# Kernel optimization log

Hardware: AMD Instinct MI355X
Metric: run time of the kernel (lower is better)

The kernel has to match this reference:

```python
import jax, jax.numpy as jnp
import numpy as np

G = 5000      # n_genes (nodes)
IN = 64       # in_dim
D = 128       # embed_dims
E = 240000    # edges (before self-loops)
SLOPE = 0.2   # leakyrelu_slope (outer) and GATv2 internal negative_slope (PyG default 0.2)


def setup_inputs() -> dict:
    key = jax.random.key(0)
    ks = jax.random.split(key, 12)
    s = 0.05
    return {
        "x": jax.random.normal(ks[0], (G, IN), jnp.float32),
        "edge_index": jax.random.randint(ks[1], (2, E), 0, G, jnp.int64),
        # per-gene input linears: n_genes independent Linear(in_dim -> embed_dims)
        "W_in": jax.random.normal(ks[2], (G, IN, D), jnp.float32) * s,
        "b_in": jnp.zeros((G, D), jnp.float32),
        # GATv2Conv params (heads=1): lin_l, lin_r, att, bias
        "W_l": jax.random.normal(ks[3], (D, D), jnp.float32) * s,
        "b_l": jnp.zeros((D,), jnp.float32),
        "W_r": jax.random.normal(ks[4], (D, D), jnp.float32) * s,
        "b_r": jnp.zeros((D,), jnp.float32),
        "att": jax.random.normal(ks[5], (D,), jnp.float32) * s,
        "bias": jnp.zeros((D,), jnp.float32),
        # output MLP: Linear(D*G -> D), Linear(D -> 1)
        "W1": jax.random.normal(ks[6], (D * G, D), jnp.float32) * 0.001,
        "b1": jnp.zeros((D,), jnp.float32),
        "W2": jax.random.normal(ks[7], (D, 1), jnp.float32) * s,
        "b2": jnp.zeros((1,), jnp.float32),
    }


def _leaky(v, slope):
    return jnp.where(v >= 0, v, slope * v)


def reference(x, edge_index, W_in, b_in, W_l, b_l, W_r, b_r, att, bias, W1, b1, W2, b2):
    # per-gene linear + relu: [G, IN] x [G, IN, D] -> [G, D]
    h = jax.nn.relu(jnp.einsum("gi,gid->gd", x, W_in) + b_in)

    # GATv2Conv (heads=1, concat, add_self_loops=True)
    xl = h @ W_l + b_l  # source-side transform [G, D]
    xr = h @ W_r + b_r  # target-side transform [G, D]
    loop = jnp.arange(G, dtype=edge_index.dtype)
    src = jnp.concatenate([edge_index[0], loop])  # [E+G]
    dst = jnp.concatenate([edge_index[1], loop])

    # attention logits per edge: att . LeakyReLU(xl[src] + xr[dst])
    e = _leaky(xl[src] + xr[dst], 0.2) @ att  # [E+G]

    # segment softmax over edges sharing a destination
    m = jax.ops.segment_max(e, dst, num_segments=G)  # [G]
    w = jnp.exp(e - m[dst])
    z = jax.ops.segment_sum(w, dst, num_segments=G)  # [G]
    alpha = w / z[dst]  # every node has a self-loop, z > 0

    # scatter-aggregate weighted messages
    out = jax.ops.segment_sum(alpha[:, None] * xl[src], dst, num_segments=G) + bias  # [G, D]

    out = _leaky(out, SLOPE)
    flat = out.reshape(-1)  # [G*D]
    h1 = jax.nn.relu(flat @ W1 + b1)
    return h1 @ W2 + b2  # [1]
```

## Files before the change

### kernel.cpp

```cpp
#include <hip/hip_runtime.h>
#include <math.h>

#define G 5000
#define IN 64
#define D 128
#define E 240000
#define EG (E + G)
#define SLOPE 0.2f
#define GD (G * D)
#define CAP 128
#define NB_M 1250
#define NB_PG 1250
#define NB_H 240
#define NB_X 1250

__device__ __forceinline__ float leaky(float v) { return v >= 0.f ? v : SLOPE * v; }

__global__ __launch_bounds__(256) void k_fuseA(const float* __restrict__ x,
                                               const float* __restrict__ Win,
                                               const float* __restrict__ bin,
                                               float* __restrict__ h,
                                               const int* __restrict__ srcA,
                                               const int* __restrict__ dstA,
                                               int* __restrict__ cnt,
                                               int* __restrict__ ssrc,
                                               float* __restrict__ outz) {
    if (blockIdx.x == 0 && threadIdx.x == 0) *outz = 0.f;
    if (blockIdx.x < NB_PG) {
        int g = (blockIdx.x * 256 + threadIdx.x) >> 6;
        int lane = threadIdx.x & 63;
        if (g >= G) return;
        float xv = x[g * IN + lane];
        const float* W = Win + (size_t)g * IN * D + lane * 2;
        float2 acc = *(const float2*)(bin + g * D + lane * 2);
#pragma unroll
        for (int i = 0; i < IN; ++i) {
            float xi = __shfl(xv, i);
            float2 w2 = *(const float2*)(W + (size_t)i * D);
            acc.x = fmaf(xi, w2.x, acc.x);
            acc.y = fmaf(xi, w2.y, acc.y);
        }
        float2 o = { fmaxf(acc.x, 0.f), fmaxf(acc.y, 0.f) };
        *(float2*)(h + g * D + lane * 2) = o;
    } else {
        int base = ((blockIdx.x - NB_PG) * 256 + threadIdx.x) * 4;
        if (base >= EG) return;
        if (base + 4 <= E) {
            int4 s4 = *(const int4*)(srcA + base);
            int4 d4 = *(const int4*)(dstA + base);
            int p;
            p = atomicAdd(&cnt[d4.x], 1); if (p < CAP) ssrc[d4.x * CAP + p] = s4.x;
            p = atomicAdd(&cnt[d4.y], 1); if (p < CAP) ssrc[d4.y * CAP + p] = s4.y;
            p = atomicAdd(&cnt[d4.z], 1); if (p < CAP) ssrc[d4.z * CAP + p] = s4.z;
            p = atomicAdd(&cnt[d4.w], 1); if (p < CAP) ssrc[d4.w * CAP + p] = s4.w;
        } else {
            for (int kk = 0; kk < 4; ++kk) {
                int i = base + kk;
                if (i < EG) {
                    int s, t;
                    if (i < E) { s = srcA[i]; t = dstA[i]; }
                    else { s = i - E; t = s; }
                    int p = atomicAdd(&cnt[t], 1);
                    if (p < CAP) ssrc[t * CAP + p] = s;
                }
            }
        }
    }
}

__global__ __launch_bounds__(256) void k_xlxr3(const float* __restrict__ h,
                                               const float* __restrict__ Wl,
                                               const float* __restrict__ bl,
                                               const float* __restrict__ Wr,
                                               const float* __restrict__ br,
                                               float* __restrict__ xl,
                                               float* __restrict__ xr) {
    int g0 = blockIdx.x * 4;
    int tid = threadIdx.x;
    int half = tid >> 7;
    int col = tid & 127;
    const float* W = half ? Wr : Wl;
    const float* bb = half ? br : bl;
    float* o = half ? xr : xl;
    const float* h0p = h + (size_t)(g0 + 0) * D;
    const float* h1p = h + (size_t)(g0 + 1) * D;
    const float* h2p = h + (size_t)(g0 + 2) * D;
    const float* h3p = h + (size_t)(g0 + 3) * D;
    float b = bb[col];
    float acc0 = b, acc1 = b, acc2 = b, acc3 = b;
#pragma unroll 8
    for (int k4 = 0; k4 < 32; ++k4) {
        int k = k4 * 4;
        float4 hv0 = *(const float4*)(h0p + k);
        float4 hv1 = *(const float4*)(h1p + k);
        float4 hv2 = *(const float4*)(h2p + k);
        float4 hv3 = *(const float4*)(h3p + k);
        float w0 = W[(size_t)(k + 0) * D + col];
        float w1 = W[(size_t)(k + 1) * D + col];
        float w2 = W[(size_t)(k + 2) * D + col];
        float w3 = W[(size_t)(k + 3) * D + col];
        acc0 = fmaf(hv0.x, w0, acc0); acc0 = fmaf(hv0.y, w1, acc0);
        acc0 = fmaf(hv0.z, w2, acc0); acc0 = fmaf(hv0.w, w3, acc0);
        acc1 = fmaf(hv1.x, w0, acc1); acc1 = fmaf(hv1.y, w1, acc1);
        acc1 = fmaf(hv1.z, w2, acc1); acc1 = fmaf(hv1.w, w3, acc1);
        acc2 = fmaf(hv2.x, w0, acc2); acc2 = fmaf(hv2.y, w1, acc2);
        acc2 = fmaf(hv2.z, w2, acc2); acc2 = fmaf(hv2.w, w3, acc2);
        acc3 = fmaf(hv3.x, w0, acc3); acc3 = fmaf(hv3.y, w1, acc3);
        acc3 = fmaf(hv3.z, w2, acc3); acc3 = fmaf(hv3.w, w3, acc3);
    }
    o[(size_t)(g0 + 0) * D + col] = acc0;
    o[(size_t)(g0 + 1) * D + col] = acc1;
    o[(size_t)(g0 + 2) * D + col] = acc2;
    o[(size_t)(g0 + 3) * D + col] = acc3;
}

__global__ __launch_bounds__(256) void k_aggmlp(const int* __restrict__ cnt,
                                                const int* __restrict__ ssrc,
                                                const float* __restrict__ xl,
                                                const float* __restrict__ xr,
                                                const float* __restrict__ att,
                                                const float* __restrict__ bias,
                                                const float* __restrict__ W1,
                                                float* __restrict__ partials) {
    int wid = threadIdx.x >> 6;
    int lane = threadIdx.x & 63;
    int t = __builtin_amdgcn_readfirstlane(blockIdx.x * 4 + wid);
    __shared__ float2 red[4][64];
    int lane2 = lane * 2;
    float2 a  = *(const float2*)(att + lane2);
    float2 r2 = *(const float2*)(xr + (size_t)t * D + lane2);
    int deg = cnt[t]; if (deg > CAP) deg = CAP;
    const int* srow = ssrc + t * CAP;
    float2 acc = { 0.f, 0.f };
    float z = 0.f;
    for (int base = 0; base < deg; base += 64) {
        int nv = deg - base; if (nv > 64) nv = 64;
        int sv = srow[base + (lane < nv ? lane : nv - 1)];
        int e = 0;
        for (; e + 4 <= nv; e += 4) {
            int s0 = __shfl(sv, e), s1 = __shfl(sv, e + 1);
            int s2 = __shfl(sv, e + 2), s3 = __shfl(sv, e + 3);
            float2 l0 = *(const float2*)(xl + (size_t)s0 * D + lane2);
            float2 l1 = *(const float2*)(xl + (size_t)s1 * D + lane2);
            float2 l2 = *(const float2*)(xl + (size_t)s2 * D + lane2);
            float2 l3 = *(const float2*)(xl + (size_t)s3 * D + lane2);
            float v0 = leaky(l0.x + r2.x) * a.x + leaky(l0.y + r2.y) * a.y;
            float v1 = leaky(l1.x + r2.x) * a.x + leaky(l1.y + r2.y) * a.y;
            float v2 = leaky(l2.x + r2.x) * a.x + leaky(l2.y + r2.y) * a.y;
            float v3 = leaky(l3.x + r2.x) * a.x + leaky(l3.y + r2.y) * a.y;
#pragma unroll
            for (int off = 32; off; off >>= 1) {
                v0 += __shfl_xor(v0, off);
                v1 += __shfl_xor(v1, off);
                v2 += __shfl_xor(v2, off);
                v3 += __shfl_xor(v3, off);
            }
            float w0 = expf(v0), w1 = expf(v1), w2 = expf(v2), w3 = expf(v3);
            z += (w0 + w1) + (w2 + w3);
            acc.x = fmaf(w0, l0.x, acc.x); acc.y = fmaf(w0, l0.y, acc.y);
            acc.x = fmaf(w1, l1.x, acc.x); acc.y = fmaf(w1, l1.y, acc.y);
            acc.x = fmaf(w2, l2.x, acc.x); acc.y = fmaf(w2, l2.y, acc.y);
            acc.x = fmaf(w3, l3.x, acc.x); acc.y = fmaf(w3, l3.y, acc.y);
        }
        for (; e < nv; ++e) {
            int s = __shfl(sv, e);
            float2 l = *(const float2*)(xl + (size_t)s * D + lane2);
            float v = leaky(l.x + r2.x) * a.x + leaky(l.y + r2.y) * a.y;
#pragma unroll
            for (int off = 32; off; off >>= 1) v += __shfl_xor(v, off);
            float w = expf(v);
            z += w;
            acc.x = fmaf(w, l.x, acc.x);
            acc.y = fmaf(w, l.y, acc.y);
        }
    }
    float inv = 1.f / z;
    float2 bv = *(const float2*)(bias + lane2);
    float2 o = { leaky(acc.x * inv + bv.x), leaky(acc.y * inv + bv.y) };

    const float* W1p = W1 + (size_t)t * D * D + lane2;
    float2 m = { 0.f, 0.f };
#pragma unroll 8
    for (int dp = 0; dp < 64; ++dp) {
        float fx = __shfl(o.x, dp);
        float fy = __shfl(o.y, dp);
        float2 wa = *(const float2*)(W1p + (size_t)(2 * dp) * D);
        float2 wb = *(const float2*)(W1p + (size_t)(2 * dp + 1) * D);
        m.x = fmaf(fx, wa.x, m.x); m.y = fmaf(fx, wa.y, m.y);
        m.x = fmaf(fy, wb.x, m.x); m.y = fmaf(fy, wb.y, m.y);
    }
    red[wid][lane] = m;
    __syncthreads();
    if (wid == 0) {
        float2 s0 = red[0][lane], s1 = red[1][lane], s2 = red[2][lane], s3 = red[3][lane];
        float2 s = { s0.x + s1.x + s2.x + s3.x, s0.y + s1.y + s2.y + s3.y };
        *(float2*)(partials + (size_t)blockIdx.x * D + lane2) = s;
    }
}

__global__ __launch_bounds__(1024) void k_final8(const float* __restrict__ partials,
                                                 const float* __restrict__ b1,
                                                 const float* __restrict__ W2,
                                                 const float* __restrict__ b2,
                                                 float* __restrict__ out) {
    int tid = threadIdx.x;
    int rg = tid >> 4;
    int cl = tid & 15;
    int c = blockIdx.x * 16 + cl;
    float s = 0.f;
    for (int r = rg; r < NB_M; r += 64) s += partials[(size_t)r * D + c];
    __shared__ float red[64][16];
    red[rg][cl] = s;
    __syncthreads();
    if (tid < 128) {
        int cc = tid & 15, seg = tid >> 4;
        float t2 = red[seg * 8][cc];
        for (int m = 1; m < 8; ++m) t2 += red[seg * 8 + m][cc];
        red[seg * 8][cc] = t2;
    }
    __syncthreads();
    if (tid < 16) {
        float tot = 0.f;
        for (int m = 0; m < 8; ++m) tot += red[m * 8][tid];
        float h1 = fmaxf(tot + b1[blockIdx.x * 16 + tid], 0.f);
        red[0][tid] = h1 * W2[blockIdx.x * 16 + tid];
    }
    __syncthreads();
    if (tid == 0) {
        float o = 0.f;
        for (int m = 0; m < 16; ++m) o += red[0][m];
        if (blockIdx.x == 0) o += b2[0];
        atomicAdd(out, o);
    }
}

extern "C" void kernel_launch(void* const* d_in, const int* in_sizes, int n_in,
                              void* d_out, int out_size, void* d_ws, size_t ws_size,
                              hipStream_t stream) {
    const float* x    = (const float*)d_in[0];
    const int*   ei   = (const int*)d_in[1];
    const float* Win  = (const float*)d_in[2];
    const float* bin  = (const float*)d_in[3];
    const float* Wl   = (const float*)d_in[4];
    const float* bl   = (const float*)d_in[5];
    const float* Wr   = (const float*)d_in[6];
    const float* br   = (const float*)d_in[7];
    const float* att  = (const float*)d_in[8];
    const float* bias = (const float*)d_in[9];
    const float* W1   = (const float*)d_in[10];
    const float* b1   = (const float*)d_in[11];
    const float* W2   = (const float*)d_in[12];
    const float* b2   = (const float*)d_in[13];
    float* out = (float*)d_out;

    float* ws       = (float*)d_ws;
    float* h        = ws;
    float* xl       = h  + GD;
    float* xr       = xl + GD;
    float* partials = xr + GD;
    int*   ssrc     = (int*)(partials + (size_t)NB_M * D);
    int*   cnt      = ssrc + (size_t)G * CAP;

    const int* srcA = ei;
    const int* dstA = ei + E;

    hipMemsetAsync(cnt, 0, G * sizeof(int), stream);
    k_fuseA<<<NB_PG + NB_H, 256, 0, stream>>>(x, Win, bin, h, srcA, dstA, cnt, ssrc, out);
    k_xlxr3<<<NB_X, 256, 0, stream>>>(h, Wl, bl, Wr, br, xl, xr);
    k_aggmlp<<<NB_M, 256, 0, stream>>>(cnt, ssrc, xl, xr, att, bias, W1, partials);
    k_final8<<<8, 1024, 0, stream>>>(partials, b1, W2, b2, out);
}
```

Before: 140.9 us.

## Split each node's edge aggregation across a full block and prefetch W1 into registers

Launches one block per node instead of one wave per node, giving each wave up to 64 of the node's edges and combining the partial softmax sums and accumulators through shared memory. Each wave loads its 32 rows of W1 into registers at the start, so the large W1 stream overlaps with the edge gather. The W1 product is split across waves by row, and a per-node partial vector is written out. This raises parallelism and memory-level concurrency, at the cost of more registers, extra block syncs and a larger partials buffer that the final reduction must sum over all nodes.

```diff
diff --git a/kernel.cpp b/kernel.cpp
--- a/kernel.cpp
+++ b/kernel.cpp
@@ -9,7 +9,6 @@
 #define SLOPE 0.2f
 #define GD (G * D)
 #define CAP 128
-#define NB_M 1250
 #define NB_PG 1250
 #define NB_H 240
 #define NB_X 1250
@@ -114,26 +113,33 @@
     o[(size_t)(g0 + 3) * D + col] = acc3;
 }
 
-__global__ __launch_bounds__(256) void k_aggmlp(const int* __restrict__ cnt,
-                                                const int* __restrict__ ssrc,
-                                                const float* __restrict__ xl,
-                                                const float* __restrict__ xr,
-                                                const float* __restrict__ att,
-                                                const float* __restrict__ bias,
-                                                const float* __restrict__ W1,
-                                                float* __restrict__ partials) {
+__global__ __launch_bounds__(256) void k_aggmlp2(const int* __restrict__ cnt,
+                                                 const int* __restrict__ ssrc,
+                                                 const float* __restrict__ xl,
+                                                 const float* __restrict__ xr,
+                                                 const float* __restrict__ att,
+                                                 const float* __restrict__ bias,
+                                                 const float* __restrict__ W1,
+                                                 float* __restrict__ partials) {
     int wid = threadIdx.x >> 6;
     int lane = threadIdx.x & 63;
-    int t = __builtin_amdgcn_readfirstlane(blockIdx.x * 4 + wid);
-    __shared__ float2 red[4][64];
+    int t = blockIdx.x;
     int lane2 = lane * 2;
+
+    const float* W1base = W1 + ((size_t)t * D + wid * 32) * D + lane2;
+    float2 w1reg[32];
+#pragma unroll
+    for (int r = 0; r < 32; ++r)
+        w1reg[r] = *(const float2*)(W1base + (size_t)r * D);
+
     float2 a  = *(const float2*)(att + lane2);
     float2 r2 = *(const float2*)(xr + (size_t)t * D + lane2);
     int deg = cnt[t]; if (deg > CAP) deg = CAP;
     const int* srow = ssrc + t * CAP;
     float2 acc = { 0.f, 0.f };
     float z = 0.f;
-    for (int base = 0; base < deg; base += 64) {
+    int base = wid * 64;
+    if (base < deg) {
         int nv = deg - base; if (nv > 64) nv = 64;
         int sv = srow[base + (lane < nv ? lane : nv - 1)];
         int e = 0;
@@ -174,27 +180,34 @@
             acc.y = fmaf(w, l.y, acc.y);
         }
     }
-    float inv = 1.f / z;
+
+    __shared__ float2 red[4][64];
+    __shared__ float zs[4];
+    red[wid][lane] = acc;
+    if (lane == 0) zs[wid] = z;
+    __syncthreads();
+    float2 s0 = red[0][lane], s1 = red[1][lane], s2 = red[2][lane], s3 = red[3][lane];
+    float2 atot = { s0.x + s1.x + s2.x + s3.x, s0.y + s1.y + s2.y + s3.y };
+    float zt = zs[0] + zs[1] + zs[2] + zs[3];
+    float inv = 1.f / zt;
     float2 bv = *(const float2*)(bias + lane2);
-    float2 o = { leaky(acc.x * inv + bv.x), leaky(acc.y * inv + bv.y) };
-
-    const float* W1p = W1 + (size_t)t * D * D + lane2;
+    float2 o = { leaky(atot.x * inv + bv.x), leaky(atot.y * inv + bv.y) };
+
     float2 m = { 0.f, 0.f };
-#pragma unroll 8
-    for (int dp = 0; dp < 64; ++dp) {
-        float fx = __shfl(o.x, dp);
-        float fy = __shfl(o.y, dp);
-        float2 wa = *(const float2*)(W1p + (size_t)(2 * dp) * D);
-        float2 wb = *(const float2*)(W1p + (size_t)(2 * dp + 1) * D);
-        m.x = fmaf(fx, wa.x, m.x); m.y = fmaf(fx, wa.y, m.y);
-        m.x = fmaf(fy, wb.x, m.x); m.y = fmaf(fy, wb.y, m.y);
-    }
+#pragma unroll
+    for (int rp = 0; rp < 16; ++rp) {
+        float fx = __shfl(o.x, wid * 16 + rp);
+        float fy = __shfl(o.y, wid * 16 + rp);
+        m.x = fmaf(fx, w1reg[2 * rp].x, m.x);     m.y = fmaf(fx, w1reg[2 * rp].y, m.y);
+        m.x = fmaf(fy, w1reg[2 * rp + 1].x, m.x); m.y = fmaf(fy, w1reg[2 * rp + 1].y, m.y);
+    }
+    __syncthreads();
     red[wid][lane] = m;
     __syncthreads();
     if (wid == 0) {
-        float2 s0 = red[0][lane], s1 = red[1][lane], s2 = red[2][lane], s3 = red[3][lane];
-        float2 s = { s0.x + s1.x + s2.x + s3.x, s0.y + s1.y + s2.y + s3.y };
-        *(float2*)(partials + (size_t)blockIdx.x * D + lane2) = s;
+        float2 m0 = red[0][lane], m1 = red[1][lane], m2 = red[2][lane], m3 = red[3][lane];
+        float2 s = { m0.x + m1.x + m2.x + m3.x, m0.y + m1.y + m2.y + m3.y };
+        *(float2*)(partials + (size_t)t * D + lane2) = s;
     }
 }
 
@@ -208,7 +221,7 @@
     int cl = tid & 15;
     int c = blockIdx.x * 16 + cl;
     float s = 0.f;
-    for (int r = rg; r < NB_M; r += 64) s += partials[(size_t)r * D + c];
+    for (int r = rg; r < G; r += 64) s += partials[(size_t)r * D + c];
     __shared__ float red[64][16];
     red[rg][cl] = s;
     __syncthreads();
@@ -258,7 +271,7 @@
     float* xl       = h  + GD;
     float* xr       = xl + GD;
     float* partials = xr + GD;
-    int*   ssrc     = (int*)(partials + (size_t)NB_M * D);
+    int*   ssrc     = (int*)(partials + (size_t)GD);
     int*   cnt      = ssrc + (size_t)G * CAP;
 
     const int* srcA = ei;
@@ -267,6 +280,6 @@
     hipMemsetAsync(cnt, 0, G * sizeof(int), stream);
     k_fuseA<<<NB_PG + NB_H, 256, 0, stream>>>(x, Win, bin, h, srcA, dstA, cnt, ssrc, out);
     k_xlxr3<<<NB_X, 256, 0, stream>>>(h, Wl, bl, Wr, br, xl, xr);
-    k_aggmlp<<<NB_M, 256, 0, stream>>>(cnt, ssrc, xl, xr, att, bias, W1, partials);
+    k_aggmlp2<<<G, 256, 0, stream>>>(cnt, ssrc, xl, xr, att, bias, W1, partials);
     k_final8<<<8, 1024, 0, stream>>>(partials, b1, W2, b2, out);
 }
```

New measurement: 184.6 us. 1.31x slower.

## Split aggregation: precompute first half of nodes in separate kernel

Applied to the files above, without the earlier changes.

The GATv2 attention aggregation for the first 2500 nodes moves into a new kernel that writes its features to a workspace buffer. The fused aggregation+W1 kernel then reads those features and only does the gather and softmax for the second half. The intent is to shorten the combined kernel, where the gather latency and the W1 streaming compete, and to balance work across waves. The cost is an extra launch and an extra 2.5 MB write and read of intermediate features.

```diff
diff --git a/kernel.cpp b/kernel.cpp
--- a/kernel.cpp
+++ b/kernel.cpp
@@ -9,12 +9,73 @@
 #define SLOPE 0.2f
 #define GD (G * D)
 #define CAP 128
+#define HALF 2500
 #define NB_M 1250
 #define NB_PG 1250
 #define NB_H 240
 #define NB_X 1250
 
 __device__ __forceinline__ float leaky(float v) { return v >= 0.f ? v : SLOPE * v; }
+
+__device__ __forceinline__ float2 agg_butterfly(int t, int lane, int lane2,
+                                                const int* __restrict__ cnt,
+                                                const int* __restrict__ ssrc,
+                                                const float* __restrict__ xl,
+                                                const float* __restrict__ xr,
+                                                const float* __restrict__ att,
+                                                const float* __restrict__ bias) {
+    float2 a  = *(const float2*)(att + lane2);
+    float2 r2 = *(const float2*)(xr + (size_t)t * D + lane2);
+    int deg = cnt[t]; if (deg > CAP) deg = CAP;
+    const int* srow = ssrc + t * CAP;
+    float2 acc = { 0.f, 0.f };
+    float z = 0.f;
+    for (int base = 0; base < deg; base += 64) {
+        int nv = deg - base; if (nv > 64) nv = 64;
+        int sv = srow[base + (lane < nv ? lane : nv - 1)];
+        int e = 0;
+        for (; e + 4 <= nv; e += 4) {
+            int s0 = __shfl(sv, e), s1 = __shfl(sv, e + 1);
+            int s2 = __shfl(sv, e + 2), s3 = __shfl(sv, e + 3);
+            float2 l0 = *(const float2*)(xl + (size_t)s0 * D + lane2);
+            float2 l1 = *(const float2*)(xl + (size_t)s1 * D + lane2);
+            float2 l2 = *(const float2*)(xl + (size_t)s2 * D + lane2);
+            float2 l3 = *(const float2*)(xl + (size_t)s3 * D + lane2);
+            float v0 = leaky(l0.x + r2.x) * a.x + leaky(l0.y + r2.y) * a.y;
+            float v1 = leaky(l1.x + r2.x) * a.x + leaky(l1.y + r2.y) * a.y;
+            float v2 = leaky(l2.x + r2.x) * a.x + leaky(l2.y + r2.y) * a.y;
+            float v3 = leaky(l3.x + r2.x) * a.x + leaky(l3.y + r2.y) * a.y;
+#pragma unroll
+            for (int off = 32; off; off >>= 1) {
+                v0 += __shfl_xor(v0, off);
+                v1 += __shfl_xor(v1, off);
+                v2 += __shfl_xor(v2, off);
+                v3 += __shfl_xor(v3, off);
+            }
+            float w0 = expf(v0), w1 = expf(v1), w2 = expf(v2), w3 = expf(v3);
+            z += (w0 + w1) + (w2 + w3);
+            acc.x = fmaf(w0, l0.x, acc.x); acc.y = fmaf(w0, l0.y, acc.y);
+            acc.x = fmaf(w1, l1.x, acc.x); acc.y = fmaf(w1, l1.y, acc.y);
+            acc.x = fmaf(w2, l2.x, acc.x); acc.y = fmaf(w2, l2.y, acc.y);
+            acc.x = fmaf(w3, l3.x, acc.x); acc.y = fmaf(w3, l3.y, acc.y);
+        }
+        for (; e < nv; ++e) {
+            int s = __shfl(sv, e);
+            float2 l = *(const float2*)(xl + (size_t)s * D + lane2);
+            float v = leaky(l.x + r2.x) * a.x + leaky(l.y + r2.y) * a.y;
+#pragma unroll
+            for (int off = 32; off; off >>= 1) v += __shfl_xor(v, off);
+            float w = expf(v);
+            z += w;
+            acc.x = fmaf(w, l.x, acc.x);
+            acc.y = fmaf(w, l.y, acc.y);
+        }
+    }
+    float inv = 1.f / z;
+    float2 bv = *(const float2*)(bias + lane2);
+    float2 o = { leaky(acc.x * inv + bv.x), leaky(acc.y * inv + bv.y) };
+    return o;
+}
 
 __global__ __launch_bounds__(256) void k_fuseA(const float* __restrict__ x,
                                                const float* __restrict__ Win,
@@ -114,69 +175,41 @@
     o[(size_t)(g0 + 3) * D + col] = acc3;
 }
 
-__global__ __launch_bounds__(256) void k_aggmlp(const int* __restrict__ cnt,
-                                                const int* __restrict__ ssrc,
-                                                const float* __restrict__ xl,
-                                                const float* __restrict__ xr,
-                                                const float* __restrict__ att,
-                                                const float* __restrict__ bias,
-                                                const float* __restrict__ W1,
-                                                float* __restrict__ partials) {
+__global__ __launch_bounds__(256) void k_agg(const int* __restrict__ cnt,
+                                             const int* __restrict__ ssrc,
+                                             const float* __restrict__ xl,
+                                             const float* __restrict__ xr,
+                                             const float* __restrict__ att,
+                                             const float* __restrict__ bias,
+                                             float* __restrict__ f) {
+    int t = (blockIdx.x * 256 + threadIdx.x) >> 6;
+    int lane = threadIdx.x & 63;
+    if (t >= HALF) return;
+    float2 o = agg_butterfly(t, lane, lane * 2, cnt, ssrc, xl, xr, att, bias);
+    *(float2*)(f + (size_t)t * D + lane * 2) = o;
+}
+
+__global__ __launch_bounds__(256) void k_aggmlp5(const int* __restrict__ cnt,
+                                                 const int* __restrict__ ssrc,
+                                                 const float* __restrict__ xl,
+                                                 const float* __restrict__ xr,
+                                                 const float* __restrict__ att,
+                                                 const float* __restrict__ bias,
+                                                 const float* __restrict__ f,
+                                                 const float* __restrict__ W1,
+                                                 float* __restrict__ partials) {
     int wid = threadIdx.x >> 6;
     int lane = threadIdx.x & 63;
     int t = __builtin_amdgcn_readfirstlane(blockIdx.x * 4 + wid);
     __shared__ float2 red[4][64];
     int lane2 = lane * 2;
-    float2 a  = *(const float2*)(att + lane2);
-    float2 r2 = *(const float2*)(xr + (size_t)t * D + lane2);
-    int deg = cnt[t]; if (deg > CAP) deg = CAP;
-    const int* srow = ssrc + t * CAP;
-    float2 acc = { 0.f, 0.f };
-    float z = 0.f;
-    for (int base = 0; base < deg; base += 64) {
-        int nv = deg - base; if (nv > 64) nv = 64;
-        int sv = srow[base + (lane < nv ? lane : nv - 1)];
-        int e = 0;
-        for (; e + 4 <= nv; e += 4) {
-            int s0 = __shfl(sv, e), s1 = __shfl(sv, e + 1);
-            int s2 = __shfl(sv, e + 2), s3 = __shfl(sv, e + 3);
-            float2 l0 = *(const float2*)(xl + (size_t)s0 * D + lane2);
-            float2 l1 = *(const float2*)(xl + (size_t)s1 * D + lane2);
-            float2 l2 = *(const float2*)(xl + (size_t)s2 * D + lane2);
-            float2 l3 = *(const float2*)(xl + (size_t)s3 * D + lane2);
-            float v0 = leaky(l0.x + r2.x) * a.x + leaky(l0.y + r2.y) * a.y;
-            float v1 = leaky(l1.x + r2.x) * a.x + leaky(l1.y + r2.y) * a.y;
-            float v2 = leaky(l2.x + r2.x) * a.x + leaky(l2.y + r2.y) * a.y;
-            float v3 = leaky(l3.x + r2.x) * a.x + leaky(l3.y + r2.y) * a.y;
-#pragma unroll
-            for (int off = 32; off; off >>= 1) {
-                v0 += __shfl_xor(v0, off);
-                v1 += __shfl_xor(v1, off);
-                v2 += __shfl_xor(v2, off);
-                v3 += __shfl_xor(v3, off);
-            }
-            float w0 = expf(v0), w1 = expf(v1), w2 = expf(v2), w3 = expf(v3);
-            z += (w0 + w1) + (w2 + w3);
-            acc.x = fmaf(w0, l0.x, acc.x); acc.y = fmaf(w0, l0.y, acc.y);
-            acc.x = fmaf(w1, l1.x, acc.x); acc.y = fmaf(w1, l1.y, acc.y);
-            acc.x = fmaf(w2, l2.x, acc.x); acc.y = fmaf(w2, l2.y, acc.y);
-            acc.x = fmaf(w3, l3.x, acc.x); acc.y = fmaf(w3, l3.y, acc.y);
-        }
-        for (; e < nv; ++e) {
-            int s = __shfl(sv, e);
-            float2 l = *(const float2*)(xl + (size_t)s * D + lane2);
-            float v = leaky(l.x + r2.x) * a.x + leaky(l.y + r2.y) * a.y;
-#pragma unroll
-            for (int off = 32; off; off >>= 1) v += __shfl_xor(v, off);
-            float w = expf(v);
-            z += w;
-            acc.x = fmaf(w, l.x, acc.x);
-            acc.y = fmaf(w, l.y, acc.y);
-        }
-    }
-    float inv = 1.f / z;
-    float2 bv = *(const float2*)(bias + lane2);
-    float2 o = { leaky(acc.x * inv + bv.x), leaky(acc.y * inv + bv.y) };
+
+    float2 o;
+    if (t < HALF) {
+        o = *(const float2*)(f + (size_t)t * D + lane2);
+    } else {
+        o = agg_butterfly(t, lane, lane2, cnt, ssrc, xl, xr, att, bias);
+    }
 
     const float* W1p = W1 + (size_t)t * D * D + lane2;
     float2 m = { 0.f, 0.f };
@@ -257,7 +290,8 @@
     float* h        = ws;
     float* xl       = h  + GD;
     float* xr       = xl + GD;
-    float* partials = xr + GD;
+    float* f        = xr + GD;
+    float* partials = f  + GD;
     int*   ssrc     = (int*)(partials + (size_t)NB_M * D);
     int*   cnt      = ssrc + (size_t)G * CAP;
 
@@ -267,6 +301,7 @@
     hipMemsetAsync(cnt, 0, G * sizeof(int), stream);
     k_fuseA<<<NB_PG + NB_H, 256, 0, stream>>>(x, Win, bin, h, srcA, dstA, cnt, ssrc, out);
     k_xlxr3<<<NB_X, 256, 0, stream>>>(h, Wl, bl, Wr, br, xl, xr);
-    k_aggmlp<<<NB_M, 256, 0, stream>>>(cnt, ssrc, xl, xr, att, bias, W1, partials);
+    k_agg<<<(HALF * 64) / 256, 256, 0, stream>>>(cnt, ssrc, xl, xr, att, bias, f);
+    k_aggmlp5<<<NB_M, 256, 0, stream>>>(cnt, ssrc, xl, xr, att, bias, f, W1, partials);
     k_final8<<<8, 1024, 0, stream>>>(partials, b1, W2, b2, out);
 }
```

After: 157.5 us. 11.7% more time.
